# Kernel tuning notes

Hardware: AMD Instinct MI355X
Metric: run time of the kernel (lower is better)

The kernel has to match this reference:

```python
import jax, jax.numpy as jnp
import numpy as np
from jax import lax

B, S, I, H, L = 64, 512, 512, 512, 2


def setup_inputs() -> dict:
    key = jax.random.key(0)
    ks = jax.random.split(key, 5)
    s = 1.0 / np.sqrt(H)
    return {
        "x": jax.random.normal(ks[0], (B, S, I), dtype=jnp.float32),
        "W_ih": jax.random.uniform(ks[1], (H, I), jnp.float32, -s, s),
        "b_ih": jax.random.uniform(ks[2], (H,), jnp.float32, -s, s),
        "W_hh": jax.random.uniform(ks[3], (H, H), jnp.float32, -s, s),
        "b_hh": jax.random.uniform(ks[4], (H,), jnp.float32, -s, s),
        "num_layers": L,
    }


def reference(x, W_ih, b_ih, W_hh, b_hh, num_layers):
    # Faithful to the torch module: a single shared RNNCell applied to
    # h of shape [B, L, H]; the input projection [B, H] broadcasts over L.
    batch = x.shape[0]
    h0 = jnp.zeros((batch, num_layers, W_hh.shape[0]), dtype=x.dtype)
    # Precompute the input projection for all timesteps (one big GEMM).
    xa = jnp.einsum("bsi,hi->bsh", x, W_ih) + b_ih  # [B, S, H]
    xa_t = jnp.swapaxes(xa, 0, 1)  # [S, B, H]

    def step(h, x_t):
        # h: [B, L, H], x_t: [B, H]
        h_new = jnp.tanh(x_t[:, None, :] + jnp.einsum("blh,gh->blg", h, W_hh) + b_hh)
        return h_new, h_new

    h_last, hs = lax.scan(step, h0, xa_t)
    y = jnp.swapaxes(hs, 0, 1)  # [B, S, L, H]
    return y, h_last
```

## Files before the change

kernel.cpp:

```cpp
#include <hip/hip_runtime.h>
#include <stdint.h>

typedef __attribute__((ext_vector_type(8))) short short8;
typedef __attribute__((ext_vector_type(4))) float f32x4;

struct alignas(16) I4 { int x, y, z, w; };
struct alignas(8)  U2 { unsigned x, y; };
struct alignas(16) F4 { float x, y, z, w; };

__device__ __forceinline__ unsigned short f2bf(float f) {
  unsigned u = __builtin_bit_cast(unsigned, f);
  u += 0x7FFFu + ((u >> 16) & 1u);
  return (unsigned short)(u >> 16);
}
__device__ __forceinline__ float bf2f(unsigned short h) {
  unsigned u = ((unsigned)h) << 16;
  return __builtin_bit_cast(float, u);
}
__device__ __forceinline__ float fast_tanh(float x) {
  float a = fabsf(x);
  float e = __expf(2.0f * a);
  float r = 1.0f - 2.0f / (e + 1.0f);
  return copysignf(r, x);
}

#define XA_OFF   0
#define WIH_OFF  33554432
#define WHH_OFF  (33554432 + 524288)
#define HBUF_OFF (33554432 + 1048576)
#define FLG_OFF  (33554432 + 1048576 + 262144)
#define YSIZE    33554432ull

__global__ __launch_bounds__(256) void prep_kernel(
    const float* __restrict__ Wih, const float* __restrict__ Whh,
    unsigned short* __restrict__ WihB, unsigned short* __restrict__ WhhB,
    float* __restrict__ hbuf, int* __restrict__ flg) {
  int t = blockIdx.x * 256 + threadIdx.x;
  WihB[t] = f2bf(Wih[t]);
  WhhB[t] = f2bf(Whh[t]);
  if (t < 4 * 2 * 16 * 512) hbuf[t] = 0.0f;
  if (t < 4 * 512 * 8) flg[t] = 0;
}

#define G1S 40
__global__ __launch_bounds__(256) void gemm1_kernel(
    const float* __restrict__ x, const unsigned short* __restrict__ WihB,
    const float* __restrict__ bih, const float* __restrict__ bhh,
    unsigned short* __restrict__ xa) {
  __shared__ alignas(16) unsigned short Alds[128 * G1S];
  const int wg = blockIdx.x;
  const int nt = wg & 3, mt = wg >> 2;
  const int tid = threadIdx.x;
  const int wave = tid >> 6, lane = tid & 63;
  const int wm = wave & 1, wn = wave >> 1;
  const int l15 = lane & 15, quad = lane >> 4;

  f32x4 acc[4][4] = {};

  const int arow = tid >> 1, ahalf = tid & 1;
  const float* aptr = x + (size_t)(mt * 128 + arow) * 512 + ahalf * 16;
  unsigned short* awr = Alds + arow * G1S + ahalf * 16;
  const int nbase = nt * 128 + wn * 64;

  for (int ks = 0; ks < 16; ++ks) {
    const F4* ap = (const F4*)(aptr + ks * 32);
#pragma unroll
    for (int j = 0; j < 4; ++j) {
      F4 v = ap[j];
      U2 u;
      u.x = (unsigned)f2bf(v.x) | ((unsigned)f2bf(v.y) << 16);
      u.y = (unsigned)f2bf(v.z) | ((unsigned)f2bf(v.w) << 16);
      *(U2*)(awr + j * 4) = u;
    }
    __syncthreads();

    short8 bfrag[4];
#pragma unroll
    for (int ni = 0; ni < 4; ++ni) {
      const int n = nbase + ni * 16 + l15;
      bfrag[ni] = __builtin_bit_cast(
          short8, *(const I4*)(WihB + (size_t)n * 512 + ks * 32 + quad * 8));
    }
    short8 afrag[4];
#pragma unroll
    for (int mi = 0; mi < 4; ++mi) {
      const unsigned short* ard = Alds + (wm * 64 + mi * 16 + l15) * G1S + quad * 8;
      afrag[mi] = __builtin_bit_cast(short8, *(const I4*)ard);
    }
#pragma unroll
    for (int mi = 0; mi < 4; ++mi)
#pragma unroll
      for (int ni = 0; ni < 4; ++ni)
        acc[mi][ni] = __builtin_amdgcn_mfma_f32_16x16x32_bf16(
            afrag[mi], bfrag[ni], acc[mi][ni], 0, 0, 0);
    __syncthreads();
  }

#pragma unroll
  for (int ni = 0; ni < 4; ++ni) {
    const int n = nbase + ni * 16 + l15;
    const float bias = bih[n] + bhh[n];
#pragma unroll
    for (int mi = 0; mi < 4; ++mi) {
#pragma unroll
      for (int r = 0; r < 4; ++r) {
        int m = mt * 128 + wm * 64 + mi * 16 + quad * 4 + r;
        int b = m >> 9, s = m & 511;
        xa[(size_t)(s * 64 + b) * 512 + n] = f2bf(acc[mi][ni][r] + bias);
      }
    }
  }
}

#define HS 520
#define PLANE (16 * HS)
__global__ __launch_bounds__(256) void rnn_kernel(
    const unsigned short* __restrict__ xa, const unsigned short* __restrict__ WhhB,
    float* __restrict__ hbuf, int* __restrict__ flg, float* __restrict__ out) {
  __shared__ alignas(16) unsigned short hlds[2 * PLANE];
  const int wg = blockIdx.x;
  const int group = wg & 3;
  const int slice = wg >> 2;
  const int tid = threadIdx.x;
  const int wave = tid >> 6, lane = tid & 63;
  const int l15 = lane & 15, quad = lane >> 4;
  const int gcol = slice * 64 + wave * 16 + l15;
  const int seqbase = group * 16;

  short8 bfrag[16];
#pragma unroll
  for (int kt = 0; kt < 16; ++kt)
    bfrag[kt] = __builtin_bit_cast(
        short8, *(const I4*)(WhhB + (size_t)gcol * 512 + kt * 32 + quad * 8));

  float* hb0 = hbuf + group * (2 * 16 * 512);
  int* flg_g = flg + group * 512 * 8;

  const int srow = tid >> 4;
  const int c15 = tid & 15;

  for (int t = 0; t < 512; ++t) {
    if (t > 0) {
      const int* fp = flg_g + (t - 1) * 8 + (lane & 7);
      for (;;) {
        int v = (lane < 8)
            ? __hip_atomic_load(fp, __ATOMIC_RELAXED, __HIP_MEMORY_SCOPE_AGENT)
            : 1;
        if (__all(v != 0)) break;
        __builtin_amdgcn_s_sleep(1);
      }
    }

    const unsigned short* xrow = xa + ((size_t)t * 64 + seqbase) * 512 + gcol;
    float xv[4];
#pragma unroll
    for (int r = 0; r < 4; ++r) xv[r] = bf2f(xrow[(quad * 4 + r) * 512]);

    {
      const float* src = hb0 + (t & 1) * (16 * 512) + srow * 512;
      unsigned short* dst = hlds + srow * HS;
#pragma unroll
      for (int jj = 0; jj < 4; ++jj) {
        const int c = jj * 16 + c15;
        const float* s8 = src + c * 8;
        float vs[8];
#pragma unroll
        for (int e = 0; e < 8; ++e)
          vs[e] = __hip_atomic_load(s8 + e, __ATOMIC_RELAXED,
                                    __HIP_MEMORY_SCOPE_AGENT);
        unsigned h[8], l[8];
#pragma unroll
        for (int e = 0; e < 8; ++e) {
          unsigned short hs = f2bf(vs[e]);
          h[e] = hs;
          l[e] = f2bf(vs[e] - bf2f(hs));
        }
        I4 hv, lv;
        hv.x = (int)(h[0] | (h[1] << 16)); hv.y = (int)(h[2] | (h[3] << 16));
        hv.z = (int)(h[4] | (h[5] << 16)); hv.w = (int)(h[6] | (h[7] << 16));
        lv.x = (int)(l[0] | (l[1] << 16)); lv.y = (int)(l[2] | (l[3] << 16));
        lv.z = (int)(l[4] | (l[5] << 16)); lv.w = (int)(l[6] | (l[7] << 16));
        *(I4*)(dst + c * 8) = hv;
        *(I4*)(dst + PLANE + c * 8) = lv;
      }
    }
    __syncthreads();

    f32x4 acch = {}, accl = {};
    const unsigned short* ard = hlds + l15 * HS + quad * 8;
#pragma unroll
    for (int kt = 0; kt < 16; ++kt) {
      short8 ah = __builtin_bit_cast(short8, *(const I4*)(ard + kt * 32));
      short8 al = __builtin_bit_cast(short8, *(const I4*)(ard + PLANE + kt * 32));
      acch = __builtin_amdgcn_mfma_f32_16x16x32_bf16(ah, bfrag[kt], acch, 0, 0, 0);
      accl = __builtin_amdgcn_mfma_f32_16x16x32_bf16(al, bfrag[kt], accl, 0, 0, 0);
    }

    float* dsth = hb0 + ((t + 1) & 1) * (16 * 512);
    float hv[4];
#pragma unroll
    for (int r = 0; r < 4; ++r) {
      const int m = quad * 4 + r;
      float pre = acch[r] + accl[r] + xv[r];
      hv[r] = fast_tanh(pre);
      __hip_atomic_store(&dsth[m * 512 + gcol], hv[r], __ATOMIC_RELAXED,
                         __HIP_MEMORY_SCOPE_AGENT);
    }
    __syncthreads();
    if (tid == 0)
      __hip_atomic_store(flg_g + t * 8 + slice, 1, __ATOMIC_RELAXED,
                         __HIP_MEMORY_SCOPE_AGENT);

#pragma unroll
    for (int r = 0; r < 4; ++r) {
      const int b = seqbase + quad * 4 + r;
      size_t ybase = ((size_t)b * 512 + t) * 1024 + gcol;
      out[ybase] = hv[r];
      out[ybase + 512] = hv[r];
      if (t == 511) {
        out[YSIZE + (size_t)b * 1024 + gcol] = hv[r];
        out[YSIZE + (size_t)b * 1024 + 512 + gcol] = hv[r];
      }
    }
  }
}

extern "C" void kernel_launch(void* const* d_in, const int* in_sizes, int n_in,
                              void* d_out, int out_size, void* d_ws, size_t ws_size,
                              hipStream_t stream) {
  (void)in_sizes; (void)n_in; (void)out_size; (void)ws_size;
  const float* x   = (const float*)d_in[0];
  const float* Wih = (const float*)d_in[1];
  const float* bih = (const float*)d_in[2];
  const float* Whh = (const float*)d_in[3];
  const float* bhh = (const float*)d_in[4];
  float* out = (float*)d_out;
  char* ws = (char*)d_ws;

  unsigned short* xaB  = (unsigned short*)(ws + XA_OFF);
  unsigned short* WihB = (unsigned short*)(ws + WIH_OFF);
  unsigned short* WhhB = (unsigned short*)(ws + WHH_OFF);
  float* hbuf          = (float*)(ws + HBUF_OFF);
  int* flg             = (int*)(ws + FLG_OFF);

  prep_kernel<<<dim3(1024), dim3(256), 0, stream>>>(Wih, Whh, WihB, WhhB, hbuf, flg);
  gemm1_kernel<<<dim3(1024), dim3(256), 0, stream>>>(x, WihB, bih, bhh, xaB);
  rnn_kernel<<<dim3(32), dim3(256), 0, stream>>>(xaB, WhhB, hbuf, flg, out);
}
```

Before: 2.897 ms.

## Switch to fp16 MFMA, single-plane h, fewer RNN blocks, staged xa prefetch

Replaces bf16 with fp16 throughout. The recurrent step now uses a single fp16 plane for h instead of the bf16 hi/lo split, which halves the MFMAs and LDS traffic per step. The RNN grid shrinks from 32 to 16 blocks, each computing 128 columns with two B fragments, so fewer blocks take part in the per-step flag barrier. The h tile in LDS uses an XOR swizzle, and xa is prefetched in chunks of four timesteps into double-buffered LDS through registers. The cost is lower precision in the recurrence (fp16 without error compensation) and more work per block.

New measurement: 3.249 ms. 1.12x slower.

```diff
diff --git a/kernel.cpp b/kernel.cpp
--- a/kernel.cpp
+++ b/kernel.cpp
@@ -1,21 +1,15 @@
 #include <hip/hip_runtime.h>
 #include <stdint.h>
 
-typedef __attribute__((ext_vector_type(8))) short short8;
+typedef _Float16 half8 __attribute__((ext_vector_type(8)));
 typedef __attribute__((ext_vector_type(4))) float f32x4;
 
 struct alignas(16) I4 { int x, y, z, w; };
 struct alignas(8)  U2 { unsigned x, y; };
 struct alignas(16) F4 { float x, y, z, w; };
 
-__device__ __forceinline__ unsigned short f2bf(float f) {
-  unsigned u = __builtin_bit_cast(unsigned, f);
-  u += 0x7FFFu + ((u >> 16) & 1u);
-  return (unsigned short)(u >> 16);
-}
-__device__ __forceinline__ float bf2f(unsigned short h) {
-  unsigned u = ((unsigned)h) << 16;
-  return __builtin_bit_cast(float, u);
+__device__ __forceinline__ unsigned short f2h(float f) {
+  return __builtin_bit_cast(unsigned short, (_Float16)f);
 }
 __device__ __forceinline__ float fast_tanh(float x) {
   float a = fabsf(x);
@@ -33,21 +27,21 @@
 
 __global__ __launch_bounds__(256) void prep_kernel(
     const float* __restrict__ Wih, const float* __restrict__ Whh,
-    unsigned short* __restrict__ WihB, unsigned short* __restrict__ WhhB,
+    _Float16* __restrict__ WihH, _Float16* __restrict__ WhhH,
     float* __restrict__ hbuf, int* __restrict__ flg) {
   int t = blockIdx.x * 256 + threadIdx.x;
-  WihB[t] = f2bf(Wih[t]);
-  WhhB[t] = f2bf(Whh[t]);
+  WihH[t] = (_Float16)Wih[t];
+  WhhH[t] = (_Float16)Whh[t];
   if (t < 4 * 2 * 16 * 512) hbuf[t] = 0.0f;
-  if (t < 4 * 512 * 8) flg[t] = 0;
+  if (t < 4 * 512 * 4) flg[t] = 0;
 }
 
 #define G1S 40
 __global__ __launch_bounds__(256) void gemm1_kernel(
-    const float* __restrict__ x, const unsigned short* __restrict__ WihB,
+    const float* __restrict__ x, const _Float16* __restrict__ WihH,
     const float* __restrict__ bih, const float* __restrict__ bhh,
-    unsigned short* __restrict__ xa) {
-  __shared__ alignas(16) unsigned short Alds[128 * G1S];
+    _Float16* __restrict__ xa) {
+  __shared__ alignas(16) _Float16 Alds[128 * G1S];
   const int wg = blockIdx.x;
   const int nt = wg & 3, mt = wg >> 2;
   const int tid = threadIdx.x;
@@ -59,7 +53,7 @@
 
   const int arow = tid >> 1, ahalf = tid & 1;
   const float* aptr = x + (size_t)(mt * 128 + arow) * 512 + ahalf * 16;
-  unsigned short* awr = Alds + arow * G1S + ahalf * 16;
+  _Float16* awr = Alds + arow * G1S + ahalf * 16;
   const int nbase = nt * 128 + wn * 64;
 
   for (int ks = 0; ks < 16; ++ks) {
@@ -68,30 +62,30 @@
     for (int j = 0; j < 4; ++j) {
       F4 v = ap[j];
       U2 u;
-      u.x = (unsigned)f2bf(v.x) | ((unsigned)f2bf(v.y) << 16);
-      u.y = (unsigned)f2bf(v.z) | ((unsigned)f2bf(v.w) << 16);
+      u.x = (unsigned)f2h(v.x) | ((unsigned)f2h(v.y) << 16);
+      u.y = (unsigned)f2h(v.z) | ((unsigned)f2h(v.w) << 16);
       *(U2*)(awr + j * 4) = u;
     }
     __syncthreads();
 
-    short8 bfrag[4];
+    half8 bfrag[4];
 #pragma unroll
     for (int ni = 0; ni < 4; ++ni) {
       const int n = nbase + ni * 16 + l15;
       bfrag[ni] = __builtin_bit_cast(
-          short8, *(const I4*)(WihB + (size_t)n * 512 + ks * 32 + quad * 8));
-    }
-    short8 afrag[4];
+          half8, *(const I4*)(WihH + (size_t)n * 512 + ks * 32 + quad * 8));
+    }
+    half8 afrag[4];
 #pragma unroll
     for (int mi = 0; mi < 4; ++mi) {
-      const unsigned short* ard = Alds + (wm * 64 + mi * 16 + l15) * G1S + quad * 8;
-      afrag[mi] = __builtin_bit_cast(short8, *(const I4*)ard);
+      const _Float16* ard = Alds + (wm * 64 + mi * 16 + l15) * G1S + quad * 8;
+      afrag[mi] = __builtin_bit_cast(half8, *(const I4*)ard);
     }
 #pragma unroll
     for (int mi = 0; mi < 4; ++mi)
 #pragma unroll
       for (int ni = 0; ni < 4; ++ni)
-        acc[mi][ni] = __builtin_amdgcn_mfma_f32_16x16x32_bf16(
+        acc[mi][ni] = __builtin_amdgcn_mfma_f32_16x16x32_f16(
             afrag[mi], bfrag[ni], acc[mi][ni], 0, 0, 0);
     __syncthreads();
   }
@@ -106,120 +100,158 @@
       for (int r = 0; r < 4; ++r) {
         int m = mt * 128 + wm * 64 + mi * 16 + quad * 4 + r;
         int b = m >> 9, s = m & 511;
-        xa[(size_t)(s * 64 + b) * 512 + n] = f2bf(acc[mi][ni][r] + bias);
-      }
-    }
-  }
-}
-
-#define HS 520
-#define PLANE (16 * HS)
-__global__ __launch_bounds__(256) void rnn_kernel(
-    const unsigned short* __restrict__ xa, const unsigned short* __restrict__ WhhB,
+        xa[(size_t)(s * 64 + b) * 512 + n] = (_Float16)(acc[mi][ni][r] + bias);
+      }
+    }
+  }
+}
+
+#define NCH 4
+__global__ __launch_bounds__(256, 1) void rnn_kernel(
+    const _Float16* __restrict__ xa, const _Float16* __restrict__ WhhH,
     float* __restrict__ hbuf, int* __restrict__ flg, float* __restrict__ out) {
-  __shared__ alignas(16) unsigned short hlds[2 * PLANE];
-  const int wg = blockIdx.x;
-  const int group = wg & 3;
-  const int slice = wg >> 2;
+  __shared__ alignas(16) _Float16 hpl[16 * 512];
+  __shared__ alignas(16) _Float16 xach[2][NCH * 16 * 128];
+  const int bid = blockIdx.x;
+  const int group = bid & 3, slice = bid >> 2;
   const int tid = threadIdx.x;
   const int wave = tid >> 6, lane = tid & 63;
   const int l15 = lane & 15, quad = lane >> 4;
-  const int gcol = slice * 64 + wave * 16 + l15;
+  const int colbase = slice * 128 + wave * 32;
   const int seqbase = group * 16;
 
-  short8 bfrag[16];
-#pragma unroll
-  for (int kt = 0; kt < 16; ++kt)
-    bfrag[kt] = __builtin_bit_cast(
-        short8, *(const I4*)(WhhB + (size_t)gcol * 512 + kt * 32 + quad * 8));
-
-  float* hb0 = hbuf + group * (2 * 16 * 512);
-  int* flg_g = flg + group * 512 * 8;
-
-  const int srow = tid >> 4;
-  const int c15 = tid & 15;
+  half8 bfrag[2][16];
+#pragma unroll
+  for (int cs = 0; cs < 2; ++cs)
+#pragma unroll
+    for (int kt = 0; kt < 16; ++kt)
+      bfrag[cs][kt] = __builtin_bit_cast(
+          half8, *(const I4*)(WhhH + (size_t)(colbase + cs * 16 + l15) * 512 +
+                              kt * 32 + quad * 8));
+
+  float* hb = hbuf + group * (2 * 8192);
+  int* flg_g = flg + group * (512 * 4);
+
+  const int srow = tid >> 4, scol = (tid & 15) * 32;
+
+  I4 xreg[4];
+#pragma unroll
+  for (int j = 0; j < 4; ++j) {
+    int slot = j * 256 + tid, s = slot >> 8, m = (slot >> 4) & 15, cb = slot & 15;
+    I4 v = *(const I4*)(xa + ((size_t)s * 64 + seqbase + m) * 512 +
+                        slice * 128 + cb * 8);
+    *(I4*)(&xach[0][(s * 16 + m) * 128 + cb * 8]) = v;
+  }
+#pragma unroll
+  for (int j = 0; j < 4; ++j) {
+    int slot = j * 256 + tid, s = slot >> 8, m = (slot >> 4) & 15, cb = slot & 15;
+    xreg[j] = *(const I4*)(xa + ((size_t)(NCH + s) * 64 + seqbase + m) * 512 +
+                           slice * 128 + cb * 8);
+  }
+#pragma unroll
+  for (int j = 0; j < 4; ++j) {
+    I4 z = {0, 0, 0, 0};
+    *(I4*)(hpl + (j * 256 + tid) * 8) = z;
+  }
+  __syncthreads();
 
   for (int t = 0; t < 512; ++t) {
     if (t > 0) {
-      const int* fp = flg_g + (t - 1) * 8 + (lane & 7);
+      const int* fp = flg_g + (t - 1) * 4 + (lane & 3);
       for (;;) {
-        int v = (lane < 8)
-            ? __hip_atomic_load(fp, __ATOMIC_RELAXED, __HIP_MEMORY_SCOPE_AGENT)
-            : 1;
+        int v = __hip_atomic_load(fp, __ATOMIC_RELAXED, __HIP_MEMORY_SCOPE_AGENT);
         if (__all(v != 0)) break;
         __builtin_amdgcn_s_sleep(1);
       }
-    }
-
-    const unsigned short* xrow = xa + ((size_t)t * 64 + seqbase) * 512 + gcol;
-    float xv[4];
-#pragma unroll
-    for (int r = 0; r < 4; ++r) xv[r] = bf2f(xrow[(quad * 4 + r) * 512]);
-
+      const float* src = hb + (t & 1) * 8192 + srow * 512 + scol;
+      float vals[32];
+#pragma unroll
+      for (int j = 0; j < 32; ++j)
+        vals[j] = __hip_atomic_load(src + j, __ATOMIC_RELAXED,
+                                    __HIP_MEMORY_SCOPE_AGENT);
+      const int xr = srow & 7;
+#pragma unroll
+      for (int jb = 0; jb < 4; ++jb) {
+        I4 pv;
+        pv.x = (int)((unsigned)f2h(vals[jb * 8 + 0]) | ((unsigned)f2h(vals[jb * 8 + 1]) << 16));
+        pv.y = (int)((unsigned)f2h(vals[jb * 8 + 2]) | ((unsigned)f2h(vals[jb * 8 + 3]) << 16));
+        pv.z = (int)((unsigned)f2h(vals[jb * 8 + 4]) | ((unsigned)f2h(vals[jb * 8 + 5]) << 16));
+        pv.w = (int)((unsigned)f2h(vals[jb * 8 + 6]) | ((unsigned)f2h(vals[jb * 8 + 7]) << 16));
+        int c8 = (scol >> 3) + jb;
+        *(I4*)(hpl + srow * 512 + ((c8 ^ xr) << 3)) = pv;
+      }
+    }
+    __syncthreads();
+
+    f32x4 acc0 = {}, acc1 = {};
     {
-      const float* src = hb0 + (t & 1) * (16 * 512) + srow * 512;
-      unsigned short* dst = hlds + srow * HS;
-#pragma unroll
-      for (int jj = 0; jj < 4; ++jj) {
-        const int c = jj * 16 + c15;
-        const float* s8 = src + c * 8;
-        float vs[8];
-#pragma unroll
-        for (int e = 0; e < 8; ++e)
-          vs[e] = __hip_atomic_load(s8 + e, __ATOMIC_RELAXED,
-                                    __HIP_MEMORY_SCOPE_AGENT);
-        unsigned h[8], l[8];
-#pragma unroll
-        for (int e = 0; e < 8; ++e) {
-          unsigned short hs = f2bf(vs[e]);
-          h[e] = hs;
-          l[e] = f2bf(vs[e] - bf2f(hs));
-        }
-        I4 hv, lv;
-        hv.x = (int)(h[0] | (h[1] << 16)); hv.y = (int)(h[2] | (h[3] << 16));
-        hv.z = (int)(h[4] | (h[5] << 16)); hv.w = (int)(h[6] | (h[7] << 16));
-        lv.x = (int)(l[0] | (l[1] << 16)); lv.y = (int)(l[2] | (l[3] << 16));
-        lv.z = (int)(l[4] | (l[5] << 16)); lv.w = (int)(l[6] | (l[7] << 16));
-        *(I4*)(dst + c * 8) = hv;
-        *(I4*)(dst + PLANE + c * 8) = lv;
-      }
-    }
-    __syncthreads();
-
-    f32x4 acch = {}, accl = {};
-    const unsigned short* ard = hlds + l15 * HS + quad * 8;
-#pragma unroll
-    for (int kt = 0; kt < 16; ++kt) {
-      short8 ah = __builtin_bit_cast(short8, *(const I4*)(ard + kt * 32));
-      short8 al = __builtin_bit_cast(short8, *(const I4*)(ard + PLANE + kt * 32));
-      acch = __builtin_amdgcn_mfma_f32_16x16x32_bf16(ah, bfrag[kt], acch, 0, 0, 0);
-      accl = __builtin_amdgcn_mfma_f32_16x16x32_bf16(al, bfrag[kt], accl, 0, 0, 0);
-    }
-
-    float* dsth = hb0 + ((t + 1) & 1) * (16 * 512);
-    float hv[4];
+      const _Float16* pl = hpl + l15 * 512;
+      const int xrr = l15 & 7;
+#pragma unroll
+      for (int kt = 0; kt < 16; ++kt) {
+        half8 a = __builtin_bit_cast(
+            half8, *(const I4*)(pl + (((kt * 4 + quad) ^ xrr) << 3)));
+        acc0 = __builtin_amdgcn_mfma_f32_16x16x32_f16(a, bfrag[0][kt], acc0, 0, 0, 0);
+        acc1 = __builtin_amdgcn_mfma_f32_16x16x32_f16(a, bfrag[1][kt], acc1, 0, 0, 0);
+      }
+    }
+
+    float* dsth = hb + ((t + 1) & 1) * 8192;
+    const _Float16* xrow = &xach[(t >> 2) & 1][(t & 3) * 16 * 128];
+    float hv0[4], hv1[4];
 #pragma unroll
     for (int r = 0; r < 4; ++r) {
       const int m = quad * 4 + r;
-      float pre = acch[r] + accl[r] + xv[r];
-      hv[r] = fast_tanh(pre);
-      __hip_atomic_store(&dsth[m * 512 + gcol], hv[r], __ATOMIC_RELAXED,
+      float p0 = acc0[r] + (float)xrow[m * 128 + wave * 32 + l15];
+      float p1 = acc1[r] + (float)xrow[m * 128 + wave * 32 + 16 + l15];
+      hv0[r] = fast_tanh(p0);
+      hv1[r] = fast_tanh(p1);
+      __hip_atomic_store(dsth + m * 512 + colbase + l15, hv0[r],
+                         __ATOMIC_RELAXED, __HIP_MEMORY_SCOPE_AGENT);
+      __hip_atomic_store(dsth + m * 512 + colbase + 16 + l15, hv1[r],
+                         __ATOMIC_RELAXED, __HIP_MEMORY_SCOPE_AGENT);
+    }
+
+    if ((t & 3) == 2) {
+      int cw = (t >> 2) + 1;
+      if (cw < 128) {
+#pragma unroll
+        for (int j = 0; j < 4; ++j) {
+          int slot = j * 256 + tid, s = slot >> 8, m = (slot >> 4) & 15, cb = slot & 15;
+          *(I4*)(&xach[cw & 1][(s * 16 + m) * 128 + cb * 8]) = xreg[j];
+        }
+        if (cw + 1 < 128) {
+          int t0 = (cw + 1) * NCH;
+#pragma unroll
+          for (int j = 0; j < 4; ++j) {
+            int slot = j * 256 + tid, s = slot >> 8, m = (slot >> 4) & 15, cb = slot & 15;
+            xreg[j] = *(const I4*)(xa + ((size_t)(t0 + s) * 64 + seqbase + m) * 512 +
+                                   slice * 128 + cb * 8);
+          }
+        }
+      }
+    }
+
+    __syncthreads();
+    if (tid == 0)
+      __hip_atomic_store(flg_g + t * 4 + slice, 1, __ATOMIC_RELAXED,
                          __HIP_MEMORY_SCOPE_AGENT);
-    }
-    __syncthreads();
-    if (tid == 0)
-      __hip_atomic_store(flg_g + t * 8 + slice, 1, __ATOMIC_RELAXED,
-                         __HIP_MEMORY_SCOPE_AGENT);
 
 #pragma unroll
     for (int r = 0; r < 4; ++r) {
-      const int b = seqbase + quad * 4 + r;
-      size_t ybase = ((size_t)b * 512 + t) * 1024 + gcol;
-      out[ybase] = hv[r];
-      out[ybase + 512] = hv[r];
+      const int m = quad * 4 + r;
+      const int b = seqbase + m;
+      size_t yb = ((size_t)b * 512 + t) * 1024 + colbase + l15;
+      out[yb] = hv0[r];
+      out[yb + 16] = hv1[r];
+      out[yb + 512] = hv0[r];
+      out[yb + 528] = hv1[r];
       if (t == 511) {
-        out[YSIZE + (size_t)b * 1024 + gcol] = hv[r];
-        out[YSIZE + (size_t)b * 1024 + 512 + gcol] = hv[r];
+        size_t hoff = YSIZE + (size_t)b * 1024 + colbase + l15;
+        out[hoff] = hv0[r];
+        out[hoff + 16] = hv1[r];
+        out[hoff + 512] = hv0[r];
+        out[hoff + 528] = hv1[r];
       }
     }
   }
@@ -237,13 +269,14 @@
   float* out = (float*)d_out;
   char* ws = (char*)d_ws;
 
-  unsigned short* xaB  = (unsigned short*)(ws + XA_OFF);
-  unsigned short* WihB = (unsigned short*)(ws + WIH_OFF);
-  unsigned short* WhhB = (unsigned short*)(ws + WHH_OFF);
-  float* hbuf          = (float*)(ws + HBUF_OFF);
-  int* flg             = (int*)(ws + FLG_OFF);
-
-  prep_kernel<<<dim3(1024), dim3(256), 0, stream>>>(Wih, Whh, WihB, WhhB, hbuf, flg);
-  gemm1_kernel<<<dim3(1024), dim3(256), 0, stream>>>(x, WihB, bih, bhh, xaB);
-  rnn_kernel<<<dim3(32), dim3(256), 0, stream>>>(xaB, WhhB, hbuf, flg, out);
-}
+  _Float16* xaH  = (_Float16*)(ws + XA_OFF);
+  _Float16* WihH = (_Float16*)(ws + WIH_OFF);
+  _Float16* WhhH = (_Float16*)(ws + WHH_OFF);
+  float* hbuf    = (float*)(ws + HBUF_OFF);
+  int* flgp      = (int*)(ws + FLG_OFF);
+
+  prep_kernel<<<dim3(1024), dim3(256), 0, stream>>>(Wih, Whh, WihH, WhhH,
+                                                    hbuf, flgp);
+  gemm1_kernel<<<dim3(1024), dim3(256), 0, stream>>>(x, WihH, bih, bhh, xaH);
+  rnn_kernel<<<dim3(16), dim3(256), 0, stream>>>(xaH, WhhH, hbuf, flgp, out);
+}
```
